# Kernel optimization log

Measured on AMD Instinct MI355X. Metric: run time of the kernel, lower is better.

## Reference

```python
import jax, jax.numpy as jnp
import numpy as np

N = 400000
NUM_OBJECTS = 80000
LOSS_WEIGHT = 1.0
EPS_W = 1e-5
EPS_A = 1e-7

X_SIGN = jnp.array([1, 1, -1, -1, 1, 1, -1, -1], dtype=jnp.float32)
Y_SIGN = jnp.array([1, -1, -1, 1, 1, -1, -1, 1], dtype=jnp.float32)
Z_SIGN = jnp.array([1, 1, 1, 1, -1, -1, -1, -1], dtype=jnp.float32)


def setup_inputs() -> dict:
    key = jax.random.key(0)
    k1, k2, k3, k4, k5, k6 = jax.random.split(key, 6)
    # 3D boxes: centers spread in front of the camera, positive sizes, yaw in [-pi, pi]
    xyz = jnp.concatenate([
        jax.random.uniform(k1, (N, 2), minval=-20.0, maxval=20.0),  # x, y lateral
        jax.random.uniform(k2, (N, 1), minval=-1.5, maxval=1.5),    # z
    ], axis=1)
    lwh = jax.random.uniform(k3, (N, 3), minval=1.0, maxval=5.0)
    yaw = jax.random.uniform(k4, (N, 1), minval=-np.pi, maxval=np.pi)
    pred_3d_bboxes = jnp.concatenate([xyz, lwh, yaw], axis=1)  # (N, 7)
    # GT 2D boxes [x1, y1, x2, y2] inside a 1600x900 image
    x1y1 = jax.random.uniform(k5, (N, 2)) * jnp.array([1200.0, 600.0])
    wh2d = jax.random.uniform(jax.random.fold_in(k5, 1), (N, 2), minval=20.0, maxval=300.0)
    gt_2d_bboxes = jnp.concatenate([x1y1, x1y1 + wh2d], axis=1)
    # Projection matrices: pinhole intrinsics * axis swap (lidar x-forward -> cam z), + tiny noise
    fx, fy, cx, cy = 1000.0, 1000.0, 800.0, 450.0
    K = jnp.array([[fx, 0.0, cx, 0.0], [0.0, fy, cy, 0.0], [0.0, 0.0, 1.0, 0.0], [0.0, 0.0, 0.0, 1.0]], dtype=jnp.float32)
    swap = jnp.array([[0.0, -1.0, 0.0, 0.0], [0.0, 0.0, -1.0, 0.0], [1.0, 0.0, 0.0, 60.0], [0.0, 0.0, 0.0, 1.0]], dtype=jnp.float32)
    base = K @ swap  # (4, 4)
    lidar2img = base[None] + 0.01 * jax.random.normal(k6, (N, 4, 4), dtype=jnp.float32)
    img_shapes = jnp.ones((N, 2), dtype=jnp.float32) * jnp.array([900.0, 1600.0], dtype=jnp.float32)
    object_ids = jax.random.randint(jax.random.fold_in(key, 7), (N,), 0, NUM_OBJECTS, dtype=jnp.int32)
    return {
        "pred_3d_bboxes": pred_3d_bboxes,
        "gt_2d_bboxes": gt_2d_bboxes,
        "lidar2img": lidar2img,
        "img_shapes": img_shapes,
        "object_ids": object_ids,
    }


def _corners_from_bboxes_3d(b):
    # b: (N, 7) -> (N, 8, 3)
    x, y, z = b[:, 0], b[:, 1], b[:, 2]
    l, w, h = b[:, 3], b[:, 4], b[:, 5]
    yaw = b[:, 6]
    xc = (l[:, None] / 2) * X_SIGN  # (N, 8)
    yc = (w[:, None] / 2) * Y_SIGN
    zc = (h[:, None] / 2) * Z_SIGN
    corners = jnp.stack([xc, yc, zc], axis=1)  # (N, 3, 8)
    c, s = jnp.cos(yaw), jnp.sin(yaw)
    zero, one = jnp.zeros_like(c), jnp.ones_like(c)
    R = jnp.stack([c, -s, zero, s, c, zero, zero, zero, one], axis=1).reshape(-1, 3, 3)
    corners = jnp.einsum('nij,njk->nik', R, corners)  # (N, 3, 8)
    center = jnp.stack([x, y, z], axis=1)[:, :, None]
    return (corners + center).transpose(0, 2, 1)  # (N, 8, 3)


def _giou(pred, gt):
    x1 = jnp.maximum(pred[:, 0], gt[:, 0])
    y1 = jnp.maximum(pred[:, 1], gt[:, 1])
    x2 = jnp.minimum(pred[:, 2], gt[:, 2])
    y2 = jnp.minimum(pred[:, 3], gt[:, 3])
    inter = jnp.maximum(x2 - x1, 0.0) * jnp.maximum(y2 - y1, 0.0)
    pa = (pred[:, 2] - pred[:, 0]) * (pred[:, 3] - pred[:, 1])
    ga = (gt[:, 2] - gt[:, 0]) * (gt[:, 3] - gt[:, 1])
    union = pa + ga - inter + EPS_A
    iou = inter / union
    cx1 = jnp.minimum(pred[:, 0], gt[:, 0])
    cy1 = jnp.minimum(pred[:, 1], gt[:, 1])
    cx2 = jnp.maximum(pred[:, 2], gt[:, 2])
    cy2 = jnp.maximum(pred[:, 3], gt[:, 3])
    c_area = jnp.maximum(cx2 - cx1, 0.0) * jnp.maximum(cy2 - cy1, 0.0) + EPS_A
    return iou - (c_area - union) / c_area


def _loss(pred_3d_bboxes, gt_2d_bboxes, lidar2img, img_shapes, object_ids):
    corners = _corners_from_bboxes_3d(pred_3d_bboxes)  # (N, 8, 3)
    ones = jnp.ones(corners.shape[:2] + (1,), dtype=corners.dtype)
    hom = jnp.concatenate([corners, ones], axis=2)  # (N, 8, 4)
    img_hom = jnp.einsum('nij,nkj->nki', lidar2img, hom)  # (N, 8, 4)
    w = jnp.maximum(img_hom[..., 2], EPS_W)  # (N, 8)
    x_img = img_hom[..., 0] / w
    y_img = img_hom[..., 1] / w
    H, W = img_shapes[:, 0], img_shapes[:, 1]
    min_x = jnp.clip(jnp.min(x_img, axis=1), 0.0, W)
    max_x = jnp.clip(jnp.max(x_img, axis=1), 0.0, W)
    min_y = jnp.clip(jnp.min(y_img, axis=1), 0.0, H)
    max_y = jnp.clip(jnp.max(y_img, axis=1), 0.0, H)
    pred_2d = jnp.stack([min_x, min_y, max_x, max_y], axis=1)  # (N, 4)
    loss = 1.0 - _giou(pred_2d, gt_2d_bboxes)  # (N,)
    # per-object mean over views, then mean over unique (present) objects
    sums = jax.ops.segment_sum(loss, object_ids, num_segments=NUM_OBJECTS)
    counts = jax.ops.segment_sum(jnp.ones_like(loss), object_ids, num_segments=NUM_OBJECTS)
    seg_mean = sums / jnp.maximum(counts, 1.0)
    present = counts > 0
    per_obj = jnp.sum(jnp.where(present, seg_mean, 0.0)) / jnp.sum(present.astype(loss.dtype))
    return LOSS_WEIGHT * per_obj


def reference(pred_3d_bboxes, gt_2d_bboxes, lidar2img, img_shapes, object_ids):
    return _loss(pred_3d_bboxes, gt_2d_bboxes, lidar2img, img_shapes, object_ids)
```

## Files before the change

### kernel.cpp

```cpp
#include <hip/hip_runtime.h>
#include <hip/hip_bf16.h>
#include <math.h>

#define NUM_OBJECTS 80000
#define EPS_W 1e-5f
#define EPS_A 1e-7f

#define LOSS_SCALE_F 262144.0f
#define INV_LOSS_SCALE_F (1.0f / 262144.0f)

#define TABLE_VEC4 20000
#define ZERO_VEC16 20001

typedef float f32x4u __attribute__((ext_vector_type(4), aligned(4)));

__global__ void zero_ws(uint4* __restrict__ ws) {
    int i = blockIdx.x * blockDim.x + threadIdx.x;
    if (i < ZERO_VEC16) ws[i] = make_uint4(0u, 0u, 0u, 0u);
}

__device__ __forceinline__ void corner_minmax(float X, float Y, float Wc,
                                              float& minx, float& maxx,
                                              float& miny, float& maxy) {
    float wd = fmaxf(Wc, EPS_W);
    float r  = __builtin_amdgcn_rcpf(wd);
    float xi = X * r;
    float yi = Y * r;
    minx = fminf(minx, xi); maxx = fmaxf(maxx, xi);
    miny = fminf(miny, yi); maxy = fmaxf(maxy, yi);
}

__global__ void __launch_bounds__(256) loss_kernel(
        const float* __restrict__ pred,
        const float* __restrict__ gt2d,
        const float* __restrict__ l2i,
        const float* __restrict__ imgsh,
        const int*   __restrict__ ids,
        unsigned int* __restrict__ table,
        int n) {
    int i = blockIdx.x * blockDim.x + threadIdx.x;
    if (i >= n) return;

    f32x4u pa = *(const f32x4u*)(pred + 7 * (size_t)i);
    f32x4u pb = *(const f32x4u*)(pred + 7 * (size_t)i + 3);
    const float4* M = (const float4*)(l2i + 16 * (size_t)i);
    float4 M0 = M[0];
    float4 M1 = M[1];
    float4 M2 = M[2];
    float4 g   = ((const float4*)gt2d)[i];
    float2 hwd = ((const float2*)imgsh)[i];
    int oid    = ids[i];

    float x = pa.x, y = pa.y, z = pa.z;
    float hl = 0.5f * pa.w, hw = 0.5f * pb.y, hh = 0.5f * pb.z;
    float yaw = pb.w;
    float s, c;
    __sincosf(yaw, &s, &c);

    float bx = M0.x * x + M0.y * y + M0.z * z + M0.w;
    float by = M1.x * x + M1.y * y + M1.z * z + M1.w;
    float bw = M2.x * x + M2.y * y + M2.z * z + M2.w;
    float Ax = (M0.x * c + M0.y * s) * hl;
    float Ay = (M1.x * c + M1.y * s) * hl;
    float Aw = (M2.x * c + M2.y * s) * hl;
    float Bx = (M0.y * c - M0.x * s) * hw;
    float By = (M1.y * c - M1.x * s) * hw;
    float Bw = (M2.y * c - M2.x * s) * hw;
    float Cx = M0.z * hh;
    float Cy = M1.z * hh;
    float Cw = M2.z * hh;

    float xp = bx + Ax, xm = bx - Ax;
    float X0 = xp + Bx, X1 = xp - Bx, X2 = xm + Bx, X3 = xm - Bx;
    float yp = by + Ay, ym = by - Ay;
    float Y0 = yp + By, Y1 = yp - By, Y2 = ym + By, Y3 = ym - By;
    float wp = bw + Aw, wm = bw - Aw;
    float W0 = wp + Bw, W1 = wp - Bw, W2 = wm + Bw, W3 = wm - Bw;

    float minx = 1e30f, maxx = -1e30f, miny = 1e30f, maxy = -1e30f;
    corner_minmax(X0 + Cx, Y0 + Cy, W0 + Cw, minx, maxx, miny, maxy);
    corner_minmax(X0 - Cx, Y0 - Cy, W0 - Cw, minx, maxx, miny, maxy);
    corner_minmax(X1 + Cx, Y1 + Cy, W1 + Cw, minx, maxx, miny, maxy);
    corner_minmax(X1 - Cx, Y1 - Cy, W1 - Cw, minx, maxx, miny, maxy);
    corner_minmax(X2 + Cx, Y2 + Cy, W2 + Cw, minx, maxx, miny, maxy);
    corner_minmax(X2 - Cx, Y2 - Cy, W2 - Cw, minx, maxx, miny, maxy);
    corner_minmax(X3 + Cx, Y3 + Cy, W3 + Cw, minx, maxx, miny, maxy);
    corner_minmax(X3 - Cx, Y3 - Cy, W3 - Cw, minx, maxx, miny, maxy);

    float H = hwd.x, W = hwd.y;
    float px1 = fminf(fmaxf(minx, 0.f), W);
    float px2 = fminf(fmaxf(maxx, 0.f), W);
    float py1 = fminf(fmaxf(miny, 0.f), H);
    float py2 = fminf(fmaxf(maxy, 0.f), H);

    float ix1 = fmaxf(px1, g.x);
    float iy1 = fmaxf(py1, g.y);
    float ix2 = fminf(px2, g.z);
    float iy2 = fminf(py2, g.w);
    float inter = fmaxf(ix2 - ix1, 0.f) * fmaxf(iy2 - iy1, 0.f);
    float pa2 = (px2 - px1) * (py2 - py1);
    float ga = (g.z - g.x) * (g.w - g.y);
    float uni = pa2 + ga - inter + EPS_A;
    float iou = inter / uni;

    float cx1 = fminf(px1, g.x);
    float cy1 = fminf(py1, g.y);
    float cx2 = fmaxf(px2, g.z);
    float cy2 = fmaxf(py2, g.w);
    float carea = fmaxf(cx2 - cx1, 0.f) * fmaxf(cy2 - cy1, 0.f) + EPS_A;
    float giou = iou - (carea - uni) / carea;
    float loss = 1.0f - giou;

    unsigned int pk = ((unsigned int)(loss * LOSS_SCALE_F + 0.5f) << 8) | 1u;
    atomicAdd(&table[oid], pk);
}

__global__ void __launch_bounds__(256) seg_reduce(
        const uint4* __restrict__ table4,
        float* __restrict__ acc,
        unsigned int* __restrict__ ticket,
        float* __restrict__ out) {
    int i = blockIdx.x * blockDim.x + threadIdx.x;
    float sm = 0.f, pr = 0.f;
    if (i < TABLE_VEC4) {
        uint4 w = table4[i];
        unsigned int c0 = w.x & 0xFFu, c1 = w.y & 0xFFu;
        unsigned int c2 = w.z & 0xFFu, c3 = w.w & 0xFFu;
        if (c0) { sm += (float)(w.x >> 8) * INV_LOSS_SCALE_F / (float)c0; pr += 1.f; }
        if (c1) { sm += (float)(w.y >> 8) * INV_LOSS_SCALE_F / (float)c1; pr += 1.f; }
        if (c2) { sm += (float)(w.z >> 8) * INV_LOSS_SCALE_F / (float)c2; pr += 1.f; }
        if (c3) { sm += (float)(w.w >> 8) * INV_LOSS_SCALE_F / (float)c3; pr += 1.f; }
    }
#pragma unroll
    for (int off = 32; off > 0; off >>= 1) {
        sm += __shfl_down(sm, off);
        pr += __shfl_down(pr, off);
    }
    __shared__ float ssm[4], spr[4];
    int lane = threadIdx.x & 63;
    int wid = threadIdx.x >> 6;
    if (lane == 0) { ssm[wid] = sm; spr[wid] = pr; }
    __syncthreads();
    if (threadIdx.x == 0) {
        float a = 0.f, b2 = 0.f;
#pragma unroll
        for (int k = 0; k < 4; ++k) { a += ssm[k]; b2 += spr[k]; }
        atomicAdd(&acc[0], a);
        atomicAdd(&acc[1], b2);
        __threadfence();
        unsigned int old = atomicAdd(ticket, 1u);
        if (old == gridDim.x - 1) {
            float s = atomicAdd(&acc[0], 0.f);
            float pcnt = atomicAdd(&acc[1], 0.f);
            out[0] = s / pcnt;
        }
    }
}

extern "C" void kernel_launch(void* const* d_in, const int* in_sizes, int n_in,
                              void* d_out, int out_size, void* d_ws, size_t ws_size,
                              hipStream_t stream) {
    const float* pred  = (const float*)d_in[0];
    const float* gt2d  = (const float*)d_in[1];
    const float* l2i   = (const float*)d_in[2];
    const float* imgsh = (const float*)d_in[3];
    const int*   ids   = (const int*)d_in[4];
    float* out = (float*)d_out;

    int n = in_sizes[0] / 7;
    int block = 256;

    unsigned int* table  = (unsigned int*)d_ws;
    float*        acc    = (float*)(table + NUM_OBJECTS);
    unsigned int* ticket = (unsigned int*)(acc + 2);

    int gridz = (ZERO_VEC16 + block - 1) / block;
    zero_ws<<<gridz, block, 0, stream>>>((uint4*)d_ws);

    int grid1 = (n + block - 1) / block;
    loss_kernel<<<grid1, block, 0, stream>>>(pred, gt2d, l2i, imgsh, ids, table, n);

    int grid2 = (TABLE_VEC4 + block - 1) / block;
    seg_reduce<<<grid2, block, 0, stream>>>((const uint4*)table, acc, ticket, out);
}
```

Baseline: 35.08 us.

## Privatize segment table per XCD to keep atomics local

Gives each XCD its own copy of the per-object packed sum/count table. The XCC id is read from a hardware register so each wave's atomics hit a table slice that stays in that die's L2, avoiding cross-die coherence traffic. The reduce kernel then sums the eight copies per object before computing the mean. In exchange it zeroes and reads eight times more workspace, and falls back to the single-table path when the workspace is too small.

```diff
diff --git a/kernel.cpp b/kernel.cpp
--- a/kernel.cpp
+++ b/kernel.cpp
@@ -3,20 +3,24 @@
 #include <math.h>
 
 #define NUM_OBJECTS 80000
+#define NXCD 8
 #define EPS_W 1e-5f
 #define EPS_A 1e-7f
 
 #define LOSS_SCALE_F 262144.0f
 #define INV_LOSS_SCALE_F (1.0f / 262144.0f)
 
-#define TABLE_VEC4 20000
-#define ZERO_VEC16 20001
+#define XCC_ID_GETREG (((4 - 1) << 11) | (0 << 6) | 20)
+
+#define TABLE_VEC4 (NUM_OBJECTS / 4)
+#define ZERO8_VEC16 (NXCD * NUM_OBJECTS / 4 + 1)
+#define ZERO1_VEC16 (NUM_OBJECTS / 4 + 1)
 
 typedef float f32x4u __attribute__((ext_vector_type(4), aligned(4)));
 
-__global__ void zero_ws(uint4* __restrict__ ws) {
+__global__ void zero_ws(uint4* __restrict__ ws, int nvec) {
     int i = blockIdx.x * blockDim.x + threadIdx.x;
-    if (i < ZERO_VEC16) ws[i] = make_uint4(0u, 0u, 0u, 0u);
+    if (i < nvec) ws[i] = make_uint4(0u, 0u, 0u, 0u);
 }
 
 __device__ __forceinline__ void corner_minmax(float X, float Y, float Wc,
@@ -30,17 +34,12 @@
     miny = fminf(miny, yi); maxy = fmaxf(maxy, yi);
 }
 
-__global__ void __launch_bounds__(256) loss_kernel(
-        const float* __restrict__ pred,
-        const float* __restrict__ gt2d,
-        const float* __restrict__ l2i,
-        const float* __restrict__ imgsh,
-        const int*   __restrict__ ids,
-        unsigned int* __restrict__ table,
-        int n) {
-    int i = blockIdx.x * blockDim.x + threadIdx.x;
-    if (i >= n) return;
-
+__device__ __forceinline__ void compute_box(
+        int i,
+        const float* __restrict__ pred, const float* __restrict__ gt2d,
+        const float* __restrict__ l2i, const float* __restrict__ imgsh,
+        const int* __restrict__ ids,
+        unsigned int& pk, int& oid) {
     f32x4u pa = *(const f32x4u*)(pred + 7 * (size_t)i);
     f32x4u pb = *(const f32x4u*)(pred + 7 * (size_t)i + 3);
     const float4* M = (const float4*)(l2i + 16 * (size_t)i);
@@ -49,7 +48,7 @@
     float4 M2 = M[2];
     float4 g   = ((const float4*)gt2d)[i];
     float2 hwd = ((const float2*)imgsh)[i];
-    int oid    = ids[i];
+    oid = ids[i];
 
     float x = pa.x, y = pa.y, z = pa.z;
     float hl = 0.5f * pa.w, hw = 0.5f * pb.y, hh = 0.5f * pb.z;
@@ -111,25 +110,54 @@
     float giou = iou - (carea - uni) / carea;
     float loss = 1.0f - giou;
 
-    unsigned int pk = ((unsigned int)(loss * LOSS_SCALE_F + 0.5f) << 8) | 1u;
-    atomicAdd(&table[oid], pk);
-}
-
+    pk = ((unsigned int)(loss * LOSS_SCALE_F + 0.5f) << 8) | 1u;
+}
+
+template <int NT>
+__global__ void __launch_bounds__(256) loss_kernel(
+        const float* __restrict__ pred, const float* __restrict__ gt2d,
+        const float* __restrict__ l2i, const float* __restrict__ imgsh,
+        const int* __restrict__ ids,
+        unsigned int* __restrict__ table, int n) {
+    int i = blockIdx.x * blockDim.x + threadIdx.x;
+    if (i >= n) return;
+    unsigned int pk; int oid;
+    compute_box(i, pred, gt2d, l2i, imgsh, ids, pk, oid);
+
+    if (NT == NXCD) {
+        unsigned int xcc = __builtin_amdgcn_s_getreg(XCC_ID_GETREG) & 7u;
+        unsigned int* p = table + (size_t)xcc * NUM_OBJECTS + oid;
+        asm volatile("global_atomic_add %0, %1, off\n\t"
+                     "s_waitcnt vmcnt(0)"
+                     :: "v"(p), "v"(pk) : "memory");
+    } else {
+        atomicAdd(&table[oid], pk);
+    }
+}
+
+template <int NT>
 __global__ void __launch_bounds__(256) seg_reduce(
-        const uint4* __restrict__ table4,
+        const unsigned int* __restrict__ table,
         float* __restrict__ acc,
         unsigned int* __restrict__ ticket,
         float* __restrict__ out) {
     int i = blockIdx.x * blockDim.x + threadIdx.x;
     float sm = 0.f, pr = 0.f;
     if (i < TABLE_VEC4) {
-        uint4 w = table4[i];
-        unsigned int c0 = w.x & 0xFFu, c1 = w.y & 0xFFu;
-        unsigned int c2 = w.z & 0xFFu, c3 = w.w & 0xFFu;
-        if (c0) { sm += (float)(w.x >> 8) * INV_LOSS_SCALE_F / (float)c0; pr += 1.f; }
-        if (c1) { sm += (float)(w.y >> 8) * INV_LOSS_SCALE_F / (float)c1; pr += 1.f; }
-        if (c2) { sm += (float)(w.z >> 8) * INV_LOSS_SCALE_F / (float)c2; pr += 1.f; }
-        if (c3) { sm += (float)(w.w >> 8) * INV_LOSS_SCALE_F / (float)c3; pr += 1.f; }
+        unsigned int sf0 = 0, sf1 = 0, sf2 = 0, sf3 = 0;
+        unsigned int c0 = 0, c1 = 0, c2 = 0, c3 = 0;
+#pragma unroll
+        for (int tt = 0; tt < NT; ++tt) {
+            uint4 w = ((const uint4*)(table + (size_t)tt * NUM_OBJECTS))[i];
+            sf0 += w.x >> 8; c0 += w.x & 0xFFu;
+            sf1 += w.y >> 8; c1 += w.y & 0xFFu;
+            sf2 += w.z >> 8; c2 += w.z & 0xFFu;
+            sf3 += w.w >> 8; c3 += w.w & 0xFFu;
+        }
+        if (c0) { sm += (float)sf0 * INV_LOSS_SCALE_F / (float)c0; pr += 1.f; }
+        if (c1) { sm += (float)sf1 * INV_LOSS_SCALE_F / (float)c1; pr += 1.f; }
+        if (c2) { sm += (float)sf2 * INV_LOSS_SCALE_F / (float)c2; pr += 1.f; }
+        if (c3) { sm += (float)sf3 * INV_LOSS_SCALE_F / (float)c3; pr += 1.f; }
     }
 #pragma unroll
     for (int off = 32; off > 0; off >>= 1) {
@@ -170,16 +198,25 @@
     int n = in_sizes[0] / 7;
     int block = 256;
 
+    bool xcd8 = ws_size >= (size_t)NXCD * NUM_OBJECTS * sizeof(unsigned int) + 16;
+    int nt = xcd8 ? NXCD : 1;
+
     unsigned int* table  = (unsigned int*)d_ws;
-    float*        acc    = (float*)(table + NUM_OBJECTS);
+    float*        acc    = (float*)(table + (size_t)nt * NUM_OBJECTS);
     unsigned int* ticket = (unsigned int*)(acc + 2);
 
-    int gridz = (ZERO_VEC16 + block - 1) / block;
-    zero_ws<<<gridz, block, 0, stream>>>((uint4*)d_ws);
+    int nvec = xcd8 ? ZERO8_VEC16 : ZERO1_VEC16;
+    int gridz = (nvec + block - 1) / block;
+    zero_ws<<<gridz, block, 0, stream>>>((uint4*)d_ws, nvec);
 
     int grid1 = (n + block - 1) / block;
-    loss_kernel<<<grid1, block, 0, stream>>>(pred, gt2d, l2i, imgsh, ids, table, n);
-
     int grid2 = (TABLE_VEC4 + block - 1) / block;
-    seg_reduce<<<grid2, block, 0, stream>>>((const uint4*)table, acc, ticket, out);
-}
+
+    if (xcd8) {
+        loss_kernel<NXCD><<<grid1, block, 0, stream>>>(pred, gt2d, l2i, imgsh, ids, table, n);
+        seg_reduce<NXCD><<<grid2, block, 0, stream>>>(table, acc, ticket, out);
+    } else {
+        loss_kernel<1><<<grid1, block, 0, stream>>>(pred, gt2d, l2i, imgsh, ids, table, n);
+        seg_reduce<1><<<grid2, block, 0, stream>>>(table, acc, ticket, out);
+    }
+}
```

After: 36.03 us. 2.7% more time.
